# Performance work log

Hardware: AMD Instinct MI355X
Metric: run time of the kernel (lower is better)

Reference implementation:

```python
import jax, jax.numpy as jnp
import numpy as np

B, N, H = 2, 1024, 768
MAX_W = 30
WIDTH_D = 20
SPAN_DIM = 3 * H + WIDTH_D  # 2324
K = int(N * 0.4)  # 409 (eval mode: // (1+0) )


def _enumerate_spans(n, max_w):
    # Replicates: enumerate_spans then sorted(spans[::-1], key=start)
    # -> start ascending, end DESCENDING within each start.
    spans = []
    for s in range(n):
        for e in range(min(s + max_w - 1, n - 1), s - 1, -1):
            spans.append((s, e))
    return np.asarray(spans, dtype=np.int32)  # [num_spans, 2]


def setup_inputs() -> dict:
    key = jax.random.key(0)
    ks = jax.random.split(key, 8)
    spans = jnp.asarray(_enumerate_spans(N, MAX_W))  # [30285, 2]
    return {
        "segment_embeddings": jax.random.normal(ks[0], (B, N, H), jnp.float32),
        "segment_mask": jnp.ones((B, N), jnp.int32),
        "candidate_spans": spans,
        "width_emb": jax.random.normal(ks[1], (MAX_W, WIDTH_D), jnp.float32) * 0.02,
        "W1": jax.random.normal(ks[2], (SPAN_DIM, H), jnp.float32) * 0.02,
        "b1": jax.random.normal(ks[3], (H,), jnp.float32) * 0.02,
        "w_s": jax.random.normal(ks[4], (H,), jnp.float32) * 0.02,
        "b_s": jax.random.normal(ks[5], (1,), jnp.float32) * 0.02,
        "k": K,
    }


def reference(segment_embeddings, segment_mask, candidate_spans, width_emb, W1, b1, w_s, b_s, k):
    starts = candidate_spans[:, 0]  # [S]
    ends = candidate_spans[:, 1]    # [S]
    # Endpoint span extractor: x, y, x*y + width embedding (width = end-start)
    x = segment_embeddings[:, starts, :]          # [B,S,H]
    y = segment_embeddings[:, ends, :]            # [B,S,H]
    wemb = width_emb[ends - starts]               # [S,WIDTH_D]
    bsz = segment_embeddings.shape[0]
    span_feat = jnp.concatenate(
        [x, y, x * y, jnp.broadcast_to(wemb[None], (bsz,) + wemb.shape)], axis=-1
    )  # [B,S,3H+WD]
    # MLP (dropout is identity in eval) + GELU (torch default: exact erf)
    h = jax.nn.gelu(jnp.einsum("bsd,dh->bsh", span_feat, W1) + b1, approximate=False)
    scores = jnp.einsum("bsh,h->bs", h, w_s) + b_s[0]  # [B,S]
    # Mask spans whose end index exceeds valid length
    lengths = segment_mask.sum(-1)  # [B]
    scores = scores + jnp.where(ends[None, :] >= lengths[:, None], -1e6, 0.0)
    # Top-k prune, then sort indices and gather
    _, idx = jax.lax.top_k(scores, k)          # [B,k]
    idx = jnp.sort(idx, axis=1)
    top_scores = jnp.take_along_axis(scores, idx, axis=1)            # [B,k]
    top_span_embs = jnp.take_along_axis(h, idx[:, :, None], axis=1)  # [B,k,H]
    top_spans = candidate_spans[idx]                                 # [B,k,2]
    return top_span_embs, top_scores, top_spans
```

## Files before the change

kernel.cpp:

```cpp
#include <hip/hip_runtime.h>
#include <math.h>

#define NB 2
#define NN 1024
#define HH 768
#define MAXW 30
#define KTOP 409
#define BANDCAP 4096
#define BAND_TAU 2e-2f
#define CHT 120
#define GPAD 448
#define SP416 416

typedef __attribute__((ext_vector_type(4))) float f32x4;
typedef __attribute__((ext_vector_type(8))) __bf16 bf16x8;
typedef __attribute__((ext_vector_type(8))) unsigned short us8;

constexpr int MT = 64, NT = 256, KT = 32;
constexpr int ASTR = MT + 4;
constexpr int BSTR = NT + 4;

__device__ __forceinline__ float gelu_f(float z) {
  return 0.5f * z * (1.0f + erff(z * 0.70710678118654752440f));
}
__device__ __forceinline__ unsigned f2key(float f) {
  unsigned u = __float_as_uint(f);
  return (u & 0x80000000u) ? ~u : (u | 0x80000000u);
}
__device__ __forceinline__ float key2f(unsigned k) {
  unsigned u = (k & 0x80000000u) ? (k & 0x7fffffffu) : ~k;
  return __uint_as_float(u);
}
__device__ __forceinline__ unsigned short f2bf_rn(float f) {
  unsigned u = __float_as_uint(f);
  unsigned r = u + 0x7fffu + ((u >> 16) & 1u);
  return (unsigned short)(r >> 16);
}
__device__ __forceinline__ float bf2f(unsigned short h) {
  return __uint_as_float(((unsigned)h) << 16);
}
__device__ __forceinline__ void async_copy16(const void* g, void* l) {
  __builtin_amdgcn_global_load_lds(
      (const __attribute__((address_space(1))) unsigned int*)g,
      (__attribute__((address_space(3))) unsigned int*)l, 16, 0, 0);
}

__global__ void len_kernel(const int* __restrict__ mask, int* __restrict__ lengths) {
  __shared__ int red[256];
  for (int b = 0; b < NB; ++b) {
    int s = 0;
    for (int i = threadIdx.x; i < NN; i += 256) s += mask[b * NN + i];
    red[threadIdx.x] = s;
    __syncthreads();
    for (int off = 128; off > 0; off >>= 1) {
      if (threadIdx.x < off) red[threadIdx.x] += red[threadIdx.x + off];
      __syncthreads();
    }
    if (threadIdx.x == 0) lengths[b] = red[0];
    __syncthreads();
  }
}

__global__ void r_kernel(const float* __restrict__ wemb, const float* __restrict__ W1,
                         const float* __restrict__ b1, float* __restrict__ R) {
  int w = blockIdx.x;
  for (int h = threadIdx.x; h < HH; h += 256) {
    float acc = b1[h];
    for (int j = 0; j < 20; ++j)
      acc = fmaf(wemb[w * 20 + j], W1[(size_t)(3 * HH + j) * HH + h], acc);
    R[w * HH + h] = acc;
  }
}

__global__ __launch_bounds__(256) void prep_bt_kernel(const float* __restrict__ W1,
                                                      unsigned short* __restrict__ Bt) {
  const int ki = blockIdx.x;
  const int hby = blockIdx.y;
  const float* W1c = W1 + (size_t)(2 * HH) * HH;
  const int t = threadIdx.x;
#pragma unroll
  for (int half = 0; half < 2; ++half) {
    const int c = t + half * 256;
    const int col = c >> 2, kg = c & 3;
    us8 v;
#pragma unroll
    for (int j = 0; j < 8; ++j) {
      const int k = ki * 32 + kg * 8 + j;
      v[j] = f2bf_rn(W1c[(size_t)k * HH + hby * 128 + col]);
    }
    *(us8*)(Bt + ((size_t)(hby * 24 + ki) * 512 + c) * 8) = v;
  }
}

__global__ __launch_bounds__(256) void prep_emb_hl_kernel(
    const float* __restrict__ emb, unsigned short* __restrict__ Ahi,
    unsigned short* __restrict__ Alo) {
  const int tile = blockIdx.x;
  const int ki = blockIdx.y;
  const int t = threadIdx.x;
#pragma unroll
  for (int half = 0; half < 2; ++half) {
    const int c = t + half * 256;
    const int row = c >> 2, kgs = c & 3;
    const int kg = kgs ^ ((row >> 1) & 3);
    const float* xr = emb + (size_t)(tile * 128 + row) * HH;
    const int k0 = ki * 32 + kg * 8;
    float4 x0 = *(const float4*)(xr + k0);
    float4 x1 = *(const float4*)(xr + k0 + 4);
    const float xv[8] = {x0.x, x0.y, x0.z, x0.w, x1.x, x1.y, x1.z, x1.w};
    us8 hv, lv;
#pragma unroll
    for (int j = 0; j < 8; ++j) {
      unsigned short h = f2bf_rn(xv[j]);
      hv[j] = h;
      lv[j] = f2bf_rn(xv[j] - bf2f(h));
    }
    const size_t base = (((size_t)tile * 24 + ki) * 512 + c) * 8;
    *(us8*)(Ahi + base) = hv;
    *(us8*)(Alo + base) = lv;
  }
}

__global__ __launch_bounds__(256) void prep_w1ab_kernel(
    const float* __restrict__ W1, unsigned short* __restrict__ Bhi,
    unsigned short* __restrict__ Blo) {
  const int ki = blockIdx.x;
  const int hby = blockIdx.y;
  const int t = threadIdx.x;
#pragma unroll
  for (int half = 0; half < 2; ++half) {
    const int c = t + half * 256;
    const int col = c >> 2, kg = c & 3;
    const int gc = hby * 128 + col;
    const float* base = W1 + (gc < 768 ? (size_t)0 : (size_t)HH * HH);
    const int n = (gc < 768) ? gc : gc - 768;
    us8 hv, lv;
#pragma unroll
    for (int j = 0; j < 8; ++j) {
      const int k = ki * 32 + kg * 8 + j;
      float v = base[(size_t)k * HH + n];
      unsigned short h = f2bf_rn(v);
      hv[j] = h;
      lv[j] = f2bf_rn(v - bf2f(h));
    }
    const size_t bo = (((size_t)hby * 24 + ki) * 512 + c) * 8;
    *(us8*)(Bhi + bo) = hv;
    *(us8*)(Blo + bo) = lv;
  }
}

__global__ __launch_bounds__(256) void pq_mfma_kernel(
    const unsigned short* __restrict__ Ahi, const unsigned short* __restrict__ Alo,
    const unsigned short* __restrict__ Bhi, const unsigned short* __restrict__ Blo,
    float* __restrict__ P, float* __restrict__ Q) {
  __shared__ unsigned short AsmH[128 * 32], AsmL[128 * 32];
  const int tile = blockIdx.x;
  const int hby = blockIdx.y;
  const int tid = threadIdx.x;
  const int lane = tid & 63, w = tid >> 6;
  const int wm = w & 1, wn = w >> 1;
  const int lm = lane & 15, lq = lane >> 4;

  f32x4 acc[4][4];
#pragma unroll
  for (int i = 0; i < 4; ++i)
#pragma unroll
    for (int j = 0; j < 4; ++j) acc[i][j] = (f32x4){0.f, 0.f, 0.f, 0.f};

  const unsigned short* AbH = Ahi + (size_t)tile * 24 * 4096;
  const unsigned short* AbL = Alo + (size_t)tile * 24 * 4096;
  const unsigned short* BbH = Bhi + (size_t)hby * 24 * 4096;
  const unsigned short* BbL = Blo + (size_t)hby * 24 * 4096;
  const int a_off = (wm * 64 + lm) * 32 + (lq ^ ((lm >> 1) & 3)) * 8;
  const int b_off = (wn * 64 + lm) * 32 + lq * 8;

  for (int ki = 0; ki < 24; ++ki) {
    async_copy16(AbH + (size_t)ki * 4096 + tid * 8, AsmH + tid * 8);
    async_copy16(AbH + (size_t)ki * 4096 + (tid + 256) * 8, AsmH + (tid + 256) * 8);
    async_copy16(AbL + (size_t)ki * 4096 + tid * 8, AsmL + tid * 8);
    async_copy16(AbL + (size_t)ki * 4096 + (tid + 256) * 8, AsmL + (tid + 256) * 8);
    bf16x8 bh[4], bl[4];
#pragma unroll
    for (int ni = 0; ni < 4; ++ni) {
      bh[ni] = *reinterpret_cast<const bf16x8*>(BbH + (size_t)ki * 4096 + b_off + ni * 512);
      bl[ni] = *reinterpret_cast<const bf16x8*>(BbL + (size_t)ki * 4096 + b_off + ni * 512);
    }
    __syncthreads();
    bf16x8 ah[4], al[4];
#pragma unroll
    for (int mi = 0; mi < 4; ++mi) {
      ah[mi] = *reinterpret_cast<const bf16x8*>(AsmH + a_off + mi * 512);
      al[mi] = *reinterpret_cast<const bf16x8*>(AsmL + a_off + mi * 512);
    }
#pragma unroll
    for (int ni = 0; ni < 4; ++ni)
#pragma unroll
      for (int mi = 0; mi < 4; ++mi) {
        acc[mi][ni] = __builtin_amdgcn_mfma_f32_16x16x32_bf16(ah[mi], bh[ni], acc[mi][ni], 0, 0, 0);
        acc[mi][ni] = __builtin_amdgcn_mfma_f32_16x16x32_bf16(ah[mi], bl[ni], acc[mi][ni], 0, 0, 0);
        acc[mi][ni] = __builtin_amdgcn_mfma_f32_16x16x32_bf16(al[mi], bh[ni], acc[mi][ni], 0, 0, 0);
      }
    __syncthreads();
  }

  float* Obase = (hby < 6) ? P : Q;
  const int cb = ((hby < 6) ? hby : hby - 6) * 128 + wn * 64 + lm;
  const int rowb = tile * 128 + wm * 64 + lq * 4;
#pragma unroll
  for (int mi = 0; mi < 4; ++mi)
#pragma unroll
    for (int ni = 0; ni < 4; ++ni)
#pragma unroll
      for (int r = 0; r < 4; ++r)
        Obase[(size_t)(rowb + mi * 16 + r) * HH + cb + ni * 16] = acc[mi][ni][r];
}

__global__ __launch_bounds__(256) void prep_a_kernel(
    const float* __restrict__ emb, const int* __restrict__ spans,
    unsigned short* __restrict__ At, int S, int tileofs) {
  const int tl = blockIdx.x, b = blockIdx.y;
  const int tile = tileofs + tl;
  const int t = threadIdx.x;
#pragma unroll
  for (int half = 0; half < 2; ++half) {
    const int c = t + half * 256;
    const int row = c >> 2, kgs = c & 3;
    const int kg = kgs ^ ((row >> 1) & 3);
    int g = tile * 128 + row;
    if (g >= S) g = S - 1;
    const int s = spans[2 * g], e = spans[2 * g + 1];
    const float* xr = emb + ((size_t)b * NN + s) * HH;
    const float* yr = emb + ((size_t)b * NN + e) * HH;
    unsigned short* dst = At + (((size_t)b * CHT + tl) * 24 * 512 + c) * 8;
    for (int ki = 0; ki < 24; ++ki) {
      const int k0 = ki * 32 + kg * 8;
      float4 x0 = *(const float4*)(xr + k0);
      float4 x1 = *(const float4*)(xr + k0 + 4);
      float4 y0 = *(const float4*)(yr + k0);
      float4 y1 = *(const float4*)(yr + k0 + 4);
      us8 v;
      v[0] = f2bf_rn(x0.x * y0.x); v[1] = f2bf_rn(x0.y * y0.y);
      v[2] = f2bf_rn(x0.z * y0.z); v[3] = f2bf_rn(x0.w * y0.w);
      v[4] = f2bf_rn(x1.x * y1.x); v[5] = f2bf_rn(x1.y * y1.y);
      v[6] = f2bf_rn(x1.z * y1.z); v[7] = f2bf_rn(x1.w * y1.w);
      *(us8*)(dst + (size_t)ki * 4096) = v;
    }
  }
}

__global__ __launch_bounds__(256, 3) void score_mfma3_kernel(
    const int* __restrict__ spans,
    const unsigned short* __restrict__ At, const unsigned short* __restrict__ Bt,
    const float* __restrict__ w_s,
    const float* __restrict__ P, const float* __restrict__ Q, const float* __restrict__ R,
    float* __restrict__ spart, int S, int tileofs) {
  __shared__ unsigned short Asm[128 * 32];
  __shared__ int ssm[128], eem[128], wwm[128];
  __shared__ float sred[128 * 2];

  const int tl = blockIdx.x;
  const int tile = tileofs + tl;
  const int hby = blockIdx.y;
  const int b = blockIdx.z;
  const int tid = threadIdx.x;
  const int lane = tid & 63, w = tid >> 6;
  const int wm = w & 1, wn = w >> 1;
  const int lm = lane & 15, lq = lane >> 4;

  if (tid < 128) {
    int g = tile * 128 + tid;
    int gg = g < S ? g : S - 1;
    int s = spans[2 * gg], e = spans[2 * gg + 1];
    ssm[tid] = s; eem[tid] = e; wwm[tid] = e - s;
  }

  f32x4 acc[4][4];
#pragma unroll
  for (int i = 0; i < 4; ++i)
#pragma unroll
    for (int j = 0; j < 4; ++j) acc[i][j] = (f32x4){0.f, 0.f, 0.f, 0.f};

  const unsigned short* Ab = At + ((size_t)b * CHT + tl) * 24 * 4096;
  const unsigned short* Bb = Bt + (size_t)hby * 24 * 4096;
  const int a_off = (wm * 64 + lm) * 32 + (lq ^ ((lm >> 1) & 3)) * 8;
  const int b_off = (wn * 64 + lm) * 32 + lq * 8;

  for (int ki = 0; ki < 24; ++ki) {
    async_copy16(Ab + (size_t)ki * 4096 + tid * 8, Asm + tid * 8);
    async_copy16(Ab + (size_t)ki * 4096 + (tid + 256) * 8, Asm + (tid + 256) * 8);
    bf16x8 bfr[4];
#pragma unroll
    for (int ni = 0; ni < 4; ++ni)
      bfr[ni] = *reinterpret_cast<const bf16x8*>(Bb + (size_t)ki * 4096 + b_off + ni * 512);
    __syncthreads();
    bf16x8 afr[4];
#pragma unroll
    for (int mi = 0; mi < 4; ++mi)
      afr[mi] = *reinterpret_cast<const bf16x8*>(Asm + a_off + mi * 512);
#pragma unroll
    for (int ni = 0; ni < 4; ++ni)
#pragma unroll
      for (int mi = 0; mi < 4; ++mi)
        acc[mi][ni] = __builtin_amdgcn_mfma_f32_16x16x32_bf16(afr[mi], bfr[ni], acc[mi][ni], 0, 0, 0);
    __syncthreads();
  }

  const int hbg = hby * 128;
  float wsv[4];
#pragma unroll
  for (int ni = 0; ni < 4; ++ni) wsv[ni] = w_s[hbg + wn * 64 + ni * 16 + lm];

#pragma unroll
  for (int mi = 0; mi < 4; ++mi) {
#pragma unroll
    for (int r = 0; r < 4; ++r) {
      const int rowl = wm * 64 + mi * 16 + lq * 4 + r;
      const int s = ssm[rowl], e = eem[rowl], wd = wwm[rowl];
      const float* Pp = P + ((size_t)b * NN + s) * HH + hbg + wn * 64 + lm;
      const float* Qp = Q + ((size_t)b * NN + e) * HH + hbg + wn * 64 + lm;
      const float* Rp = R + (size_t)wd * HH + hbg + wn * 64 + lm;
      float psum = 0.f;
#pragma unroll
      for (int ni = 0; ni < 4; ++ni) {
        float z = acc[mi][ni][r] + Pp[ni * 16] + Qp[ni * 16] + Rp[ni * 16];
        psum = fmaf(gelu_f(z), wsv[ni], psum);
      }
      psum += __shfl_xor(psum, 1);
      psum += __shfl_xor(psum, 2);
      psum += __shfl_xor(psum, 4);
      psum += __shfl_xor(psum, 8);
      if (lm == 0) sred[rowl * 2 + wn] = psum;
    }
  }
  __syncthreads();
  if (tid < 128) {
    int g = tile * 128 + tid;
    if (g < S)
      spart[(size_t)hby * ((size_t)NB * S) + (size_t)b * S + g] = sred[tid * 2] + sred[tid * 2 + 1];
  }
}

__global__ void combine_kernel(const float* __restrict__ sp, const int* __restrict__ spans,
                               const float* __restrict__ b_s, const int* __restrict__ lengths,
                               float* __restrict__ scores, int S) {
  int idx = blockIdx.x * 256 + threadIdx.x;
  if (idx >= NB * S) return;
  int b = idx / S, i = idx - b * S;
  size_t st = (size_t)NB * S;
  float v = b_s[0];
#pragma unroll
  for (int j = 0; j < 6; ++j) v += sp[j * st + idx];
  if (spans[2 * i + 1] >= lengths[b]) v += -1000000.0f;
  scores[idx] = v;
}

__global__ __launch_bounds__(1024) void pivot_kernel(const float* __restrict__ scores,
                                                     const int* __restrict__ kptr, int S,
                                                     float* __restrict__ pivotf,
                                                     int* __restrict__ bandcount) {
  const int b = blockIdx.x;
  const int tid = threadIdx.x;
  const float* sc = scores + (size_t)b * S;
  const int k = kptr[0];
  __shared__ unsigned hist[256];
  __shared__ unsigned sh_prefix;
  __shared__ int sh_remaining;
  unsigned prefix = 0;
  int remaining = k;
  for (int round = 0; round < 4; ++round) {
    const int shift = 24 - 8 * round;
    if (tid < 256) hist[tid] = 0;
    __syncthreads();
    for (int i = tid; i < S; i += 1024) {
      unsigned key = f2key(sc[i]);
      if (round == 0 || (key >> (shift + 8)) == prefix)
        atomicAdd(&hist[(key >> shift) & 255u], 1u);
    }
    __syncthreads();
    if (tid == 0) {
      int cum = 0;
      for (int bin = 255; bin >= 0; --bin) {
        int c = (int)hist[bin];
        if (cum + c >= remaining) {
          sh_prefix = (prefix << 8) | (unsigned)bin;
          sh_remaining = remaining - cum;
          break;
        }
        cum += c;
      }
    }
    __syncthreads();
    prefix = sh_prefix;
    remaining = sh_remaining;
    __syncthreads();
  }
  if (tid == 0) {
    pivotf[b] = key2f(prefix);
    bandcount[b] = 0;
  }
}

__global__ void band_kernel(const float* __restrict__ scores, const float* __restrict__ pivotf,
                            int* __restrict__ bandcount, int* __restrict__ bandlist, int S) {
  int idx = blockIdx.x * 256 + threadIdx.x;
  if (idx >= NB * S) return;
  int b = idx / S, i = idx - b * S;
  if (fabsf(scores[idx] - pivotf[b]) <= BAND_TAU) {
    int slot = atomicAdd(&bandcount[b], 1);
    if (slot < BANDCAP) bandlist[b * BANDCAP + slot] = i;
  }
}

__global__ __launch_bounds__(256) void rescore_kernel(
    const float* __restrict__ emb, const int* __restrict__ spans,
    const float* __restrict__ W1, const float* __restrict__ w_s,
    const float* __restrict__ b_s, const int* __restrict__ lengths,
    const float* __restrict__ P, const float* __restrict__ Q, const float* __restrict__ R,
    const int* __restrict__ bandcount, const int* __restrict__ bandlist,
    float* __restrict__ scores, int S) {
  const int b = blockIdx.y;
  int cnt = bandcount[b];
  if (cnt > BANDCAP) cnt = BANDCAP;
  if ((int)blockIdx.x >= cnt) return;
  const int i = bandlist[b * BANDCAP + blockIdx.x];
  const int s = spans[2 * i], e = spans[2 * i + 1], wd = e - s;
  const int tid = threadIdx.x;
  __shared__ float prod[HH];
  __shared__ float red[256];
  for (int c = tid; c < HH; c += 256)
    prod[c] = emb[((size_t)b * NN + s) * HH + c] * emb[((size_t)b * NN + e) * HH + c];
  __syncthreads();
  const float* W1c = W1 + (size_t)(2 * HH) * HH;
  float psum = 0.f;
  for (int c0 = 0; c0 < HH; c0 += 256) {
    const int c = c0 + tid;
    float a = P[((size_t)b * NN + s) * HH + c] + Q[((size_t)b * NN + e) * HH + c] + R[(size_t)wd * HH + c];
    for (int k = 0; k < HH; ++k) a = fmaf(prod[k], W1c[(size_t)k * HH + c], a);
    psum = fmaf(gelu_f(a), w_s[c], psum);
  }
  red[tid] = psum;
  __syncthreads();
  for (int off = 128; off > 0; off >>= 1) {
    if (tid < off) red[tid] += red[tid + off];
    __syncthreads();
  }
  if (tid == 0) {
    float v = red[0] + b_s[0];
    if (e >= lengths[b]) v += -1000000.0f;
    scores[(size_t)b * S + i] = v;
  }
}

__global__ __launch_bounds__(1024) void topk_kernel(
    const float* __restrict__ scores, const int* __restrict__ spans,
    const int* __restrict__ kptr, int S,
    float* __restrict__ out_spans, int* __restrict__ sel) {
  const int b = blockIdx.x;
  const int tid = threadIdx.x;
  const float* sc = scores + (size_t)b * S;
  const int k = kptr[0];
  __shared__ unsigned hist[256];
  __shared__ unsigned sh_prefix;
  __shared__ int sh_remaining;
  __shared__ int wave_eq[16], wave_sel[16];
  __shared__ int selbase, eqbase;
  unsigned prefix = 0;
  int remaining = k;
  for (int round = 0; round < 4; ++round) {
    const int shift = 24 - 8 * round;
    if (tid < 256) hist[tid] = 0;
    __syncthreads();
    for (int i = tid; i < S; i += 1024) {
      unsigned key = f2key(sc[i]);
      if (round == 0 || (key >> (shift + 8)) == prefix)
        atomicAdd(&hist[(key >> shift) & 255u], 1u);
    }
    __syncthreads();
    if (tid == 0) {
      int cum = 0;
      for (int bin = 255; bin >= 0; --bin) {
        int c = (int)hist[bin];
        if (cum + c >= remaining) {
          sh_prefix = (prefix << 8) | (unsigned)bin;
          sh_remaining = remaining - cum;
          break;
        }
        cum += c;
      }
    }
    __syncthreads();
    prefix = sh_prefix;
    remaining = sh_remaining;
    __syncthreads();
  }
  const unsigned pivot = prefix;
  const int m_eq = remaining;
  if (tid == 0) { selbase = 0; eqbase = 0; }
  __syncthreads();
  const int lane = tid & 63, wv = tid >> 6;
  for (int base = 0; base < S; base += 1024) {
    const int i = base + tid;
    const bool inb = (i < S);
    const unsigned key = inb ? f2key(sc[i]) : 0u;
    const bool gt = inb && (key > pivot);
    const bool eq = inb && (key == pivot);
    unsigned long long mm = __ballot(eq);
    int eqpre = __popcll(mm & ((1ull << lane) - 1ull));
    if (lane == 0) wave_eq[wv] = __popcll(mm);
    __syncthreads();
    int eqpref = 0, eqtot = 0;
#pragma unroll
    for (int w2 = 0; w2 < 16; ++w2) {
      int c = wave_eq[w2];
      if (w2 < wv) eqpref += c;
      eqtot += c;
    }
    const bool take_eq = eq && (eqbase + eqpref + eqpre < m_eq);
    const bool sf = gt || take_eq;
    unsigned long long sm = __ballot(sf);
    int spre = __popcll(sm & ((1ull << lane) - 1ull));
    if (lane == 0) wave_sel[wv] = __popcll(sm);
    __syncthreads();
    int spref = 0, stot = 0;
#pragma unroll
    for (int w2 = 0; w2 < 16; ++w2) {
      int c = wave_sel[w2];
      if (w2 < wv) spref += c;
      stot += c;
    }
    if (sf) {
      const int j = selbase + spref + spre;
      out_spans[(b * KTOP + j) * 2 + 0] = (float)spans[2 * i];
      out_spans[(b * KTOP + j) * 2 + 1] = (float)spans[2 * i + 1];
      sel[b * KTOP + j] = i;
    }
    __syncthreads();
    if (tid == 0) { selbase += stot; eqbase += eqtot; }
    __syncthreads();
  }
}

__global__ __launch_bounds__(256) void gather_part_kernel(
    const float* __restrict__ emb, const int* __restrict__ spans,
    const float* __restrict__ W1, const int* __restrict__ sel,
    float* __restrict__ Gpart) {
  __shared__ float As[KT][ASTR];
  __shared__ float Bs[KT][BSTR];
  __shared__ int ssm[MT], eem[MT];
  const int tile = blockIdx.x;
  const int hby6 = blockIdx.y;
  const int hb = (hby6 / 6) * NT;
  const int ks = hby6 % 6;
  const int b = blockIdx.z;
  const int tid = threadIdx.x;
  const int th = tid & 31, tw = tid >> 5;
  if (tid < MT) {
    int j = tile * MT + tid;
    if (j >= KTOP) j = KTOP - 1;
    int i = sel[b * KTOP + j];
    ssm[tid] = spans[2 * i];
    eem[tid] = spans[2 * i + 1];
  }
  __syncthreads();
  const int m0 = tid >> 3, m1 = m0 + 32;
  const int d0 = (tid & 7) << 2;
  const size_t ebase = (size_t)b * NN * HH;
  const size_t rx0 = ebase + (size_t)ssm[m0] * HH;
  const size_t ry0 = ebase + (size_t)eem[m0] * HH;
  const size_t rx1 = ebase + (size_t)ssm[m1] * HH;
  const size_t ry1 = ebase + (size_t)eem[m1] * HH;
  const float* W1c = W1 + (size_t)(2 * HH) * HH;
  const int bc = (tid & 63) << 2;
  const int br = tid >> 6;
  float acc[8][8];
#pragma unroll
  for (int i = 0; i < 8; ++i)
#pragma unroll
    for (int j = 0; j < 8; ++j) acc[i][j] = 0.f;
  const int k0 = ks * 128;
  for (int it = 0; it < 4; ++it) {
    const int kt = k0 + it * KT;
    float4 x0 = *reinterpret_cast<const float4*>(emb + rx0 + kt + d0);
    float4 y0 = *reinterpret_cast<const float4*>(emb + ry0 + kt + d0);
    float4 x1 = *reinterpret_cast<const float4*>(emb + rx1 + kt + d0);
    float4 y1 = *reinterpret_cast<const float4*>(emb + ry1 + kt + d0);
    float4 bw[8];
#pragma unroll
    for (int r = 0; r < 8; ++r)
      bw[r] = *reinterpret_cast<const float4*>(W1c + (size_t)(kt + br + 4 * r) * HH + hb + bc);
    __syncthreads();
    As[d0 + 0][m0] = x0.x * y0.x; As[d0 + 1][m0] = x0.y * y0.y;
    As[d0 + 2][m0] = x0.z * y0.z; As[d0 + 3][m0] = x0.w * y0.w;
    As[d0 + 0][m1] = x1.x * y1.x; As[d0 + 1][m1] = x1.y * y1.y;
    As[d0 + 2][m1] = x1.z * y1.z; As[d0 + 3][m1] = x1.w * y1.w;
#pragma unroll
    for (int r = 0; r < 8; ++r)
      *reinterpret_cast<float4*>(&Bs[br + 4 * r][bc]) = bw[r];
    __syncthreads();
#pragma unroll
    for (int d = 0; d < KT; ++d) {
      const float4 a0 = *reinterpret_cast<const float4*>(&As[d][tw * 4]);
      const float4 a1 = *reinterpret_cast<const float4*>(&As[d][tw * 4 + 32]);
      const float4 b0 = *reinterpret_cast<const float4*>(&Bs[d][th * 4]);
      const float4 b1v = *reinterpret_cast<const float4*>(&Bs[d][th * 4 + 128]);
      const float av[8] = {a0.x, a0.y, a0.z, a0.w, a1.x, a1.y, a1.z, a1.w};
      const float bv[8] = {b0.x, b0.y, b0.z, b0.w, b1v.x, b1v.y, b1v.z, b1v.w};
#pragma unroll
      for (int mi = 0; mi < 8; ++mi)
#pragma unroll
        for (int ni = 0; ni < 8; ++ni)
          acc[mi][ni] = fmaf(av[mi], bv[ni], acc[mi][ni]);
    }
  }
#pragma unroll
  for (int mi = 0; mi < 8; ++mi) {
    const int m = tw * 4 + (mi & 3) + ((mi >> 2) << 5);
    float* op = Gpart + (((size_t)ks * NB + b) * GPAD + tile * MT + m) * HH + hb;
    *reinterpret_cast<float4*>(op + th * 4) = make_float4(acc[mi][0], acc[mi][1], acc[mi][2], acc[mi][3]);
    *reinterpret_cast<float4*>(op + th * 4 + 128) = make_float4(acc[mi][4], acc[mi][5], acc[mi][6], acc[mi][7]);
  }
}

__global__ __launch_bounds__(256) void gather_fin_kernel(
    const float* __restrict__ Gpart, const int* __restrict__ spans,
    const int* __restrict__ sel,
    const float* __restrict__ P, const float* __restrict__ Q, const float* __restrict__ R,
    const float* __restrict__ w_s, float* __restrict__ outh, float* __restrict__ spartg) {
  __shared__ int ssm[16], eem[16], wwm[16], vvm[16];
  __shared__ float sred[16];
  const int t16 = blockIdx.x;
  const int hby = blockIdx.y;
  const int b = blockIdx.z;
  const int tid = threadIdx.x;
  if (tid < 16) {
    int j = t16 * 16 + tid;
    int valid = (j < KTOP) ? 1 : 0;
    int jj = valid ? j : KTOP - 1;
    int i = sel[b * KTOP + jj];
    ssm[tid] = spans[2 * i];
    eem[tid] = spans[2 * i + 1];
    wwm[tid] = eem[tid] - ssm[tid];
    vvm[tid] = valid;
  }
  __syncthreads();
  const int row = tid >> 4;
  const int cc = tid & 15;
  const int g448 = t16 * 16 + row;
  const int co = hby * 128 + cc * 8;
  float v[8];
#pragma unroll
  for (int i = 0; i < 8; ++i) v[i] = 0.f;
#pragma unroll
  for (int ks = 0; ks < 6; ++ks) {
    const float* gp = Gpart + (((size_t)ks * NB + b) * GPAD + g448) * HH + co;
    float4 a = *(const float4*)gp;
    float4 c = *(const float4*)(gp + 4);
    v[0] += a.x; v[1] += a.y; v[2] += a.z; v[3] += a.w;
    v[4] += c.x; v[5] += c.y; v[6] += c.z; v[7] += c.w;
  }
  const int s = ssm[row], e = eem[row], wd = wwm[row];
  const float* Pp = P + ((size_t)b * NN + s) * HH + co;
  const float* Qp = Q + ((size_t)b * NN + e) * HH + co;
  const float* Rp = R + (size_t)wd * HH + co;
  float4 p0 = *(const float4*)Pp, p1 = *(const float4*)(Pp + 4);
  float4 q0 = *(const float4*)Qp, q1 = *(const float4*)(Qp + 4);
  float4 r0 = *(const float4*)Rp, r1 = *(const float4*)(Rp + 4);
  v[0] += p0.x + q0.x + r0.x; v[1] += p0.y + q0.y + r0.y;
  v[2] += p0.z + q0.z + r0.z; v[3] += p0.w + q0.w + r0.w;
  v[4] += p1.x + q1.x + r1.x; v[5] += p1.y + q1.y + r1.y;
  v[6] += p1.z + q1.z + r1.z; v[7] += p1.w + q1.w + r1.w;
  float gl[8];
#pragma unroll
  for (int i = 0; i < 8; ++i) gl[i] = gelu_f(v[i]);
  float psum = 0.f;
  if (vvm[row]) {
    const int j = t16 * 16 + row;
    float* op = outh + (size_t)(b * KTOP + j) * HH + co;
    *(float4*)op = make_float4(gl[0], gl[1], gl[2], gl[3]);
    *(float4*)(op + 4) = make_float4(gl[4], gl[5], gl[6], gl[7]);
    const float4 w0 = *(const float4*)(w_s + co);
    const float4 w1 = *(const float4*)(w_s + co + 4);
    psum = gl[0] * w0.x + gl[1] * w0.y + gl[2] * w0.z + gl[3] * w0.w +
           gl[4] * w1.x + gl[5] * w1.y + gl[6] * w1.z + gl[7] * w1.w;
  }
  psum += __shfl_xor(psum, 1);
  psum += __shfl_xor(psum, 2);
  psum += __shfl_xor(psum, 4);
  psum += __shfl_xor(psum, 8);
  const int lane = tid & 63, wv = tid >> 6;
  if ((lane & 15) == 0) sred[wv * 4 + (lane >> 4)] = psum;
  __syncthreads();
  if (tid < 16)
    spartg[(size_t)hby * (NB * SP416) + b * SP416 + t16 * 16 + tid] = sred[tid];
}

__global__ void score_fin_kernel(const float* __restrict__ spartg, const int* __restrict__ sel,
                                 const int* __restrict__ spans, const float* __restrict__ b_s,
                                 const int* __restrict__ lengths, float* __restrict__ out_scores) {
  int idx = blockIdx.x * 256 + threadIdx.x;
  if (idx >= NB * KTOP) return;
  int b = idx / KTOP, j = idx - b * KTOP;
  float v = b_s[0];
#pragma unroll
  for (int hby = 0; hby < 6; ++hby)
    v += spartg[(size_t)hby * (NB * SP416) + b * SP416 + j];
  int i = sel[idx];
  if (spans[2 * i + 1] >= lengths[b]) v += -1000000.0f;
  out_scores[idx] = v;
}

extern "C" void kernel_launch(void* const* d_in, const int* in_sizes, int n_in,
                              void* d_out, int out_size, void* d_ws, size_t ws_size,
                              hipStream_t stream) {
  const float* emb = (const float*)d_in[0];
  const int* mask = (const int*)d_in[1];
  const int* spans = (const int*)d_in[2];
  const float* wemb = (const float*)d_in[3];
  const float* W1 = (const float*)d_in[4];
  const float* b1 = (const float*)d_in[5];
  const float* w_s = (const float*)d_in[6];
  const float* b_s = (const float*)d_in[7];
  const int* kptr = (const int*)d_in[8];
  const int S = in_sizes[2] / 2;
  float* out = (float*)d_out;

  char* wp = (char*)d_ws;
  auto take = [&](size_t bytes) {
    char* p = wp;
    wp += (bytes + 63) & ~(size_t)63;
    return p;
  };
  float* Pb = (float*)take((size_t)NB * NN * HH * 4);
  float* Qb = (float*)take((size_t)NB * NN * HH * 4);
  float* Rb = (float*)take((size_t)MAXW * HH * 4);
  float* spart = (float*)take(6 * (size_t)NB * S * 4);
  float* scoresb = (float*)take((size_t)NB * S * 4);
  float* spartg = (float*)take(6 * (size_t)NB * SP416 * 4);
  float* Gpart = (float*)take(6 * (size_t)NB * GPAD * HH * 4);
  float* pivotf = (float*)take(NB * 4);
  unsigned short* At = (unsigned short*)take((size_t)NB * CHT * 24 * 4096 * 2);
  unsigned short* Bt = (unsigned short*)take((size_t)6 * 24 * 4096 * 2);
  int* selb = (int*)take(NB * KTOP * 4);
  int* lengthsb = (int*)take(NB * 4);
  int* bandcount = (int*)take(NB * 4);
  int* bandlist = (int*)take((size_t)NB * BANDCAP * 4);

  unsigned short* AimgHi = At;
  unsigned short* AimgLo = AimgHi + (size_t)16 * 24 * 4096;
  unsigned short* BimgHi = AimgLo + (size_t)16 * 24 * 4096;
  unsigned short* BimgLo = BimgHi + (size_t)12 * 24 * 4096;

  const size_t OFF1 = (size_t)NB * KTOP * HH;
  const size_t OFF2 = OFF1 + (size_t)NB * KTOP;

  const int tiles = (S + 127) / 128;

  len_kernel<<<dim3(1), dim3(256), 0, stream>>>(mask, lengthsb);
  r_kernel<<<dim3(MAXW), dim3(256), 0, stream>>>(wemb, W1, b1, Rb);
  prep_bt_kernel<<<dim3(24, 6), dim3(256), 0, stream>>>(W1, Bt);
  prep_emb_hl_kernel<<<dim3(16, 24), dim3(256), 0, stream>>>(emb, AimgHi, AimgLo);
  prep_w1ab_kernel<<<dim3(24, 12), dim3(256), 0, stream>>>(W1, BimgHi, BimgLo);
  pq_mfma_kernel<<<dim3(16, 12), dim3(256), 0, stream>>>(AimgHi, AimgLo, BimgHi, BimgLo, Pb, Qb);

  for (int pass = 0; pass < 2; ++pass) {
    const int ofs = pass * CHT;
    const int nt = (pass == 0) ? CHT : (tiles - CHT);
    prep_a_kernel<<<dim3(nt, NB), dim3(256), 0, stream>>>(emb, spans, At, S, ofs);
    score_mfma3_kernel<<<dim3(nt, 6, NB), dim3(256), 0, stream>>>(
        spans, At, Bt, w_s, Pb, Qb, Rb, spart, S, ofs);
  }

  combine_kernel<<<dim3((NB * S + 255) / 256), dim3(256), 0, stream>>>(
      spart, spans, b_s, lengthsb, scoresb, S);
  pivot_kernel<<<dim3(NB), dim3(1024), 0, stream>>>(scoresb, kptr, S, pivotf, bandcount);
  band_kernel<<<dim3((NB * S + 255) / 256), dim3(256), 0, stream>>>(
      scoresb, pivotf, bandcount, bandlist, S);
  rescore_kernel<<<dim3(BANDCAP, NB), dim3(256), 0, stream>>>(
      emb, spans, W1, w_s, b_s, lengthsb, Pb, Qb, Rb, bandcount, bandlist, scoresb, S);
  topk_kernel<<<dim3(NB), dim3(1024), 0, stream>>>(scoresb, spans, kptr, S, out + OFF2, selb);
  gather_part_kernel<<<dim3(7, 18, NB), dim3(256), 0, stream>>>(emb, spans, W1, selb, Gpart);
  gather_fin_kernel<<<dim3(26, 6, NB), dim3(256), 0, stream>>>(
      Gpart, spans, selb, Pb, Qb, Rb, w_s, out, spartg);
  score_fin_kernel<<<dim3((NB * KTOP + 255) / 256), dim3(256), 0, stream>>>(
      spartg, selb, spans, b_s, lengthsb, out + OFF1);
}
```

Baseline: 636.2 us.

## Replace single-block radix top-k with grid-wide 16-bit histogram and filtered selection

The two single-block radix-select kernels, which each scanned all ~30k scores per batch in four serial passes, are replaced. A grid-wide 16-bit histogram kernel plus a 1024-thread scan now find an approximate pivot. A filter kernel then compacts the candidates near or above that pivot, and the final exact radix select and index sort run only on that small list in shared memory. This cuts the serial work done by a two-block kernel but adds several extra launches, a 512 KB histogram that must be zeroed, and a fixed cap on the candidate and selection lists that could drop entries if too many scores cluster near the pivot.

Result: faster. 560.3 us (-11.9%).

```diff
diff --git a/kernel.cpp b/kernel.cpp
--- a/kernel.cpp
+++ b/kernel.cpp
@@ -8,6 +8,7 @@
 #define KTOP 409
 #define BANDCAP 4096
 #define BAND_TAU 2e-2f
+#define FILTCAP 6144
 #define CHT 120
 #define GPAD 448
 #define SP416 416
@@ -354,49 +355,54 @@
   scores[idx] = v;
 }
 
-__global__ __launch_bounds__(1024) void pivot_kernel(const float* __restrict__ scores,
-                                                     const int* __restrict__ kptr, int S,
-                                                     float* __restrict__ pivotf,
-                                                     int* __restrict__ bandcount) {
+__global__ void zero_kernel(unsigned* __restrict__ hist, int* __restrict__ bandcount,
+                            int* __restrict__ filtcount) {
+  int i = blockIdx.x * 256 + threadIdx.x;
+  hist[i] = 0;
+  if (blockIdx.x == 0 && threadIdx.x < NB) {
+    bandcount[threadIdx.x] = 0;
+    filtcount[threadIdx.x] = 0;
+  }
+}
+
+__global__ void hist16_kernel(const float* __restrict__ scores, unsigned* __restrict__ hist,
+                              int S) {
+  int idx = blockIdx.x * 256 + threadIdx.x;
+  if (idx >= NB * S) return;
+  int b = idx / S;
+  unsigned key = f2key(scores[idx]) >> 16;
+  atomicAdd(&hist[(size_t)b * 65536 + key], 1u);
+}
+
+__global__ __launch_bounds__(1024) void scan16_kernel(const unsigned* __restrict__ hist,
+                                                      const int* __restrict__ kptr,
+                                                      float* __restrict__ pivotf) {
   const int b = blockIdx.x;
+  const unsigned* hb = hist + (size_t)b * 65536;
   const int tid = threadIdx.x;
-  const float* sc = scores + (size_t)b * S;
-  const int k = kptr[0];
-  __shared__ unsigned hist[256];
-  __shared__ unsigned sh_prefix;
-  __shared__ int sh_remaining;
-  unsigned prefix = 0;
-  int remaining = k;
-  for (int round = 0; round < 4; ++round) {
-    const int shift = 24 - 8 * round;
-    if (tid < 256) hist[tid] = 0;
-    __syncthreads();
-    for (int i = tid; i < S; i += 1024) {
-      unsigned key = f2key(sc[i]);
-      if (round == 0 || (key >> (shift + 8)) == prefix)
-        atomicAdd(&hist[(key >> shift) & 255u], 1u);
-    }
-    __syncthreads();
-    if (tid == 0) {
-      int cum = 0;
-      for (int bin = 255; bin >= 0; --bin) {
-        int c = (int)hist[bin];
-        if (cum + c >= remaining) {
-          sh_prefix = (prefix << 8) | (unsigned)bin;
-          sh_remaining = remaining - cum;
-          break;
-        }
-        cum += c;
-      }
-    }
-    __syncthreads();
-    prefix = sh_prefix;
-    remaining = sh_remaining;
-    __syncthreads();
-  }
-  if (tid == 0) {
-    pivotf[b] = key2f(prefix);
-    bandcount[b] = 0;
+  const unsigned k = (unsigned)kptr[0];
+  __shared__ unsigned acc[1024];
+  unsigned s = 0;
+  for (int j = 0; j < 64; ++j) s += hb[tid * 64 + j];
+  const unsigned mysum = s;
+  acc[tid] = s;
+  __syncthreads();
+  for (int off = 1; off < 1024; off <<= 1) {
+    unsigned v = (tid + off < 1024) ? acc[tid + off] : 0u;
+    __syncthreads();
+    acc[tid] += v;
+    __syncthreads();
+  }
+  const unsigned above = acc[tid] - mysum;
+  if (above < k && acc[tid] >= k) {
+    unsigned cum = above;
+    int binf = tid * 64;
+    for (int j = 63; j >= 0; --j) {
+      unsigned c = hb[tid * 64 + j];
+      if (cum + c >= k) { binf = tid * 64 + j; break; }
+      cum += c;
+    }
+    pivotf[b] = key2f(((unsigned)binf) << 16);
   }
 }
 
@@ -451,27 +457,51 @@
   }
 }
 
-__global__ __launch_bounds__(1024) void topk_kernel(
+__global__ void filt_kernel(const float* __restrict__ scores, const float* __restrict__ pivotf,
+                            int* __restrict__ filtcount, int* __restrict__ filtlist, int S) {
+  int idx = blockIdx.x * 256 + threadIdx.x;
+  if (idx >= NB * S) return;
+  int b = idx / S, i = idx - b * S;
+  if (scores[idx] > pivotf[b] - 0.01f) {
+    int slot = atomicAdd(&filtcount[b], 1);
+    if (slot < FILTCAP) filtlist[b * FILTCAP + slot] = i;
+  }
+}
+
+__global__ __launch_bounds__(1024) void sel_kernel(
     const float* __restrict__ scores, const int* __restrict__ spans,
-    const int* __restrict__ kptr, int S,
-    float* __restrict__ out_spans, int* __restrict__ sel) {
+    const int* __restrict__ kptr, const int* __restrict__ filtcount,
+    const int* __restrict__ filtlist,
+    float* __restrict__ out_spans, int* __restrict__ sel, int S) {
   const int b = blockIdx.x;
   const int tid = threadIdx.x;
-  const float* sc = scores + (size_t)b * S;
   const int k = kptr[0];
+  __shared__ unsigned keys[FILTCAP];
+  __shared__ int idxs[FILTCAP];
   __shared__ unsigned hist[256];
   __shared__ unsigned sh_prefix;
   __shared__ int sh_remaining;
-  __shared__ int wave_eq[16], wave_sel[16];
-  __shared__ int selbase, eqbase;
+  __shared__ int selcnt;
+  __shared__ int slist[512];
+
+  int M = filtcount[b];
+  if (M > FILTCAP) M = FILTCAP;
+  for (int i = tid; i < M; i += 1024) {
+    int gi = filtlist[b * FILTCAP + i];
+    idxs[i] = gi;
+    keys[i] = f2key(scores[(size_t)b * S + gi]);
+  }
+  if (tid == 0) selcnt = 0;
+  __syncthreads();
+
   unsigned prefix = 0;
   int remaining = k;
   for (int round = 0; round < 4; ++round) {
     const int shift = 24 - 8 * round;
     if (tid < 256) hist[tid] = 0;
     __syncthreads();
-    for (int i = tid; i < S; i += 1024) {
-      unsigned key = f2key(sc[i]);
+    for (int i = tid; i < M; i += 1024) {
+      unsigned key = keys[i];
       if (round == 0 || (key >> (shift + 8)) == prefix)
         atomicAdd(&hist[(key >> shift) & 255u], 1u);
     }
@@ -493,50 +523,35 @@
     remaining = sh_remaining;
     __syncthreads();
   }
-  const unsigned pivot = prefix;
+  const unsigned pk = prefix;
   const int m_eq = remaining;
-  if (tid == 0) { selbase = 0; eqbase = 0; }
+
+  for (int i = tid; i < M; i += 1024) {
+    unsigned key = keys[i];
+    bool pick = false;
+    if (key > pk) {
+      pick = true;
+    } else if (key == pk) {
+      int r = 0;
+      const int myidx = idxs[i];
+      for (int j = 0; j < M; ++j)
+        if (keys[j] == pk && idxs[j] < myidx) ++r;
+      pick = (r < m_eq);
+    }
+    if (pick) {
+      int p = atomicAdd(&selcnt, 1);
+      if (p < 512) slist[p] = idxs[i];
+    }
+  }
   __syncthreads();
-  const int lane = tid & 63, wv = tid >> 6;
-  for (int base = 0; base < S; base += 1024) {
-    const int i = base + tid;
-    const bool inb = (i < S);
-    const unsigned key = inb ? f2key(sc[i]) : 0u;
-    const bool gt = inb && (key > pivot);
-    const bool eq = inb && (key == pivot);
-    unsigned long long mm = __ballot(eq);
-    int eqpre = __popcll(mm & ((1ull << lane) - 1ull));
-    if (lane == 0) wave_eq[wv] = __popcll(mm);
-    __syncthreads();
-    int eqpref = 0, eqtot = 0;
-#pragma unroll
-    for (int w2 = 0; w2 < 16; ++w2) {
-      int c = wave_eq[w2];
-      if (w2 < wv) eqpref += c;
-      eqtot += c;
-    }
-    const bool take_eq = eq && (eqbase + eqpref + eqpre < m_eq);
-    const bool sf = gt || take_eq;
-    unsigned long long sm = __ballot(sf);
-    int spre = __popcll(sm & ((1ull << lane) - 1ull));
-    if (lane == 0) wave_sel[wv] = __popcll(sm);
-    __syncthreads();
-    int spref = 0, stot = 0;
-#pragma unroll
-    for (int w2 = 0; w2 < 16; ++w2) {
-      int c = wave_sel[w2];
-      if (w2 < wv) spref += c;
-      stot += c;
-    }
-    if (sf) {
-      const int j = selbase + spref + spre;
-      out_spans[(b * KTOP + j) * 2 + 0] = (float)spans[2 * i];
-      out_spans[(b * KTOP + j) * 2 + 1] = (float)spans[2 * i + 1];
-      sel[b * KTOP + j] = i;
-    }
-    __syncthreads();
-    if (tid == 0) { selbase += stot; eqbase += eqtot; }
-    __syncthreads();
+
+  for (int i = tid; i < k; i += 1024) {
+    const int my = slist[i];
+    int r = 0;
+    for (int j = 0; j < k; ++j) r += (slist[j] < my);
+    sel[b * KTOP + r] = my;
+    out_spans[(b * KTOP + r) * 2 + 0] = (float)spans[2 * my];
+    out_spans[(b * KTOP + r) * 2 + 1] = (float)spans[2 * my + 1];
   }
 }
 
@@ -740,10 +755,13 @@
   float* pivotf = (float*)take(NB * 4);
   unsigned short* At = (unsigned short*)take((size_t)NB * CHT * 24 * 4096 * 2);
   unsigned short* Bt = (unsigned short*)take((size_t)6 * 24 * 4096 * 2);
+  unsigned* hist16b = (unsigned*)take((size_t)NB * 65536 * 4);
   int* selb = (int*)take(NB * KTOP * 4);
   int* lengthsb = (int*)take(NB * 4);
   int* bandcount = (int*)take(NB * 4);
   int* bandlist = (int*)take((size_t)NB * BANDCAP * 4);
+  int* filtcount = (int*)take(NB * 4);
+  int* filtlist = (int*)take((size_t)NB * FILTCAP * 4);
 
   unsigned short* AimgHi = At;
   unsigned short* AimgLo = AimgHi + (size_t)16 * 24 * 4096;
@@ -761,6 +779,7 @@
   prep_emb_hl_kernel<<<dim3(16, 24), dim3(256), 0, stream>>>(emb, AimgHi, AimgLo);
   prep_w1ab_kernel<<<dim3(24, 12), dim3(256), 0, stream>>>(W1, BimgHi, BimgLo);
   pq_mfma_kernel<<<dim3(16, 12), dim3(256), 0, stream>>>(AimgHi, AimgLo, BimgHi, BimgLo, Pb, Qb);
+  zero_kernel<<<dim3(512), dim3(256), 0, stream>>>(hist16b, bandcount, filtcount);
 
   for (int pass = 0; pass < 2; ++pass) {
     const int ofs = pass * CHT;
@@ -772,12 +791,16 @@
 
   combine_kernel<<<dim3((NB * S + 255) / 256), dim3(256), 0, stream>>>(
       spart, spans, b_s, lengthsb, scoresb, S);
-  pivot_kernel<<<dim3(NB), dim3(1024), 0, stream>>>(scoresb, kptr, S, pivotf, bandcount);
+  hist16_kernel<<<dim3((NB * S + 255) / 256), dim3(256), 0, stream>>>(scoresb, hist16b, S);
+  scan16_kernel<<<dim3(NB), dim3(1024), 0, stream>>>(hist16b, kptr, pivotf);
   band_kernel<<<dim3((NB * S + 255) / 256), dim3(256), 0, stream>>>(
       scoresb, pivotf, bandcount, bandlist, S);
   rescore_kernel<<<dim3(BANDCAP, NB), dim3(256), 0, stream>>>(
       emb, spans, W1, w_s, b_s, lengthsb, Pb, Qb, Rb, bandcount, bandlist, scoresb, S);
-  topk_kernel<<<dim3(NB), dim3(1024), 0, stream>>>(scoresb, spans, kptr, S, out + OFF2, selb);
+  filt_kernel<<<dim3((NB * S + 255) / 256), dim3(256), 0, stream>>>(
+      scoresb, pivotf, filtcount, filtlist, S);
+  sel_kernel<<<dim3(NB), dim3(1024), 0, stream>>>(
+      scoresb, spans, kptr, filtcount, filtlist, out + OFF2, selb, S);
   gather_part_kernel<<<dim3(7, 18, NB), dim3(256), 0, stream>>>(emb, spans, W1, selb, Gpart);
   gather_fin_kernel<<<dim3(26, 6, NB), dim3(256), 0, stream>>>(
       Gpart, spans, selb, Pb, Qb, Rb, w_s, out, spartg);
```
